# Optimization experiments

Measured on AMD Instinct MI355X. Metric: run time of the kernel, lower is better.

## Reference

```python
import jax, jax.numpy as jnp
import numpy as np

N = 30000   # nodes per graph batch
E = 480000  # edges per graph batch
G = 64      # number of graphs
IN = 20
D = 512
H = 4
C = D // H  # 128 per-head channels
HID = 128
EPS = 1e-5


def setup_inputs() -> dict:
    key = jax.random.key(0)
    ks = jax.random.split(key, 40)
    rn = lambda k, s, sc=0.05: jax.random.normal(k, s, jnp.float32) * sc
    inp = {}
    inp["wl_x"] = jax.random.normal(ks[0], (N, IN), jnp.float32)
    inp["mt_x"] = jax.random.normal(ks[1], (N, IN), jnp.float32)
    inp["wl_edge_index"] = jax.random.randint(ks[2], (2, E), 0, N)
    inp["mt_edge_index"] = jax.random.randint(ks[3], (2, E), 0, N)
    inp["wl_batch"] = jnp.sort(jax.random.randint(ks[4], (N,), 0, G))
    inp["mt_batch"] = jnp.sort(jax.random.randint(ks[5], (N,), 0, G))
    # GIN1 MLP: 20 -> 512 -> 512
    inp["gin1_W1"] = rn(ks[6], (IN, D)); inp["gin1_b1"] = jnp.zeros((D,), jnp.float32)
    inp["gin1_W2"] = rn(ks[7], (D, D)); inp["gin1_b2"] = jnp.zeros((D,), jnp.float32)
    inp["bn1_g"] = jnp.ones((D,), jnp.float32); inp["bn1_b"] = jnp.zeros((D,), jnp.float32)
    # GIN2 MLP: 512 -> 512 -> 512
    inp["gin2_W1"] = rn(ks[8], (D, D)); inp["gin2_b1"] = jnp.zeros((D,), jnp.float32)
    inp["gin2_W2"] = rn(ks[9], (D, D)); inp["gin2_b2"] = jnp.zeros((D,), jnp.float32)
    inp["bn2_g"] = jnp.ones((D,), jnp.float32); inp["bn2_b"] = jnp.zeros((D,), jnp.float32)
    # GAT: 512 -> 4 heads x 128, concat -> 512
    inp["gat_W"] = rn(ks[10], (D, H * C))
    inp["gat_as"] = rn(ks[11], (H, C))
    inp["gat_ad"] = rn(ks[12], (H, C))
    inp["gat_bias"] = jnp.zeros((H * C,), jnp.float32)
    # fc_wl: 512 -> 512 -> BN -> ReLU -> 128
    inp["fc_W1"] = rn(ks[13], (D, D)); inp["fc_b1"] = jnp.zeros((D,), jnp.float32)
    inp["fc_bn_g"] = jnp.ones((D,), jnp.float32); inp["fc_bn_b"] = jnp.zeros((D,), jnp.float32)
    inp["fc_W2"] = rn(ks[14], (D, HID)); inp["fc_b2"] = jnp.zeros((HID,), jnp.float32)
    inp["reg_W1"] = rn(ks[15], (2 * HID, HID)); inp["reg_b1"] = jnp.zeros((HID,), jnp.float32)
    inp["reg_W2"] = rn(ks[16], (HID, 1)); inp["reg_b2"] = jnp.zeros((1,), jnp.float32)
    return inp


def _bn(h, g, b):
    m = h.mean(0)
    v = h.var(0)
    return (h - m) * jax.lax.rsqrt(v + EPS) * g + b


def reference(wl_x, mt_x, wl_edge_index, mt_edge_index, wl_batch, mt_batch,
              gin1_W1, gin1_b1, gin1_W2, gin1_b2, bn1_g, bn1_b,
              gin2_W1, gin2_b1, gin2_W2, gin2_b2, bn2_g, bn2_b,
              gat_W, gat_as, gat_ad, gat_bias,
              fc_W1, fc_b1, fc_bn_g, fc_bn_b, fc_W2, fc_b2,
              reg_W1, reg_b1, reg_W2, reg_b2):
    def branch(x, ei, batch):
        n = x.shape[0]
        src, dst = ei[0], ei[1]
        # GIN1: nn((1+eps)*x + sum_{j->i} x_j), eps=0
        agg = jax.ops.segment_sum(x[src], dst, num_segments=n)
        h = x + agg
        h = jax.nn.relu(h @ gin1_W1 + gin1_b1) @ gin1_W2 + gin1_b2
        h = jax.nn.relu(_bn(h, bn1_g, bn1_b))
        # GIN2
        agg = jax.ops.segment_sum(h[src], dst, num_segments=n)
        h2 = h + agg
        h2 = jax.nn.relu(h2 @ gin2_W1 + gin2_b1) @ gin2_W2 + gin2_b2
        h2 = jax.nn.relu(_bn(h2, bn2_g, bn2_b))
        # GAT (adds self-loops, LeakyReLU(0.2), softmax over incoming edges)
        loop = jnp.arange(n)
        s2 = jnp.concatenate([src, loop])
        d2 = jnp.concatenate([dst, loop])
        hh = (h2 @ gat_W).reshape(n, H, C)           # [n,H,C]
        a_s = (hh * gat_as).sum(-1)                  # [n,H]
        a_d = (hh * gat_ad).sum(-1)                  # [n,H]
        e = jax.nn.leaky_relu(a_s[s2] + a_d[d2], 0.2)  # [E+n,H]
        mx = jax.ops.segment_max(e, d2, num_segments=n)
        ex = jnp.exp(e - mx[d2])
        den = jax.ops.segment_sum(ex, d2, num_segments=n)
        alpha = ex / den[d2]                          # [E+n,H]
        out = jax.ops.segment_sum(hh[s2] * alpha[:, :, None], d2,
                                  num_segments=n).reshape(n, H * C) + gat_bias
        # global add pool over graphs
        g = jax.ops.segment_sum(out, batch, num_segments=G)  # [G,512]
        # shared fc head
        g = jax.nn.relu(_bn(g @ fc_W1 + fc_b1, fc_bn_g, fc_bn_b)) @ fc_W2 + fc_b2
        return g                                       # [G,128]

    xw = branch(wl_x, wl_edge_index, wl_batch)
    xm = branch(mt_x, mt_edge_index, mt_batch)
    x = jnp.concatenate([xw, xm], axis=1)             # [G,256]
    ddg = (jax.nn.relu(x @ reg_W1 + reg_b1) @ reg_W2 + reg_b2)[:, 0]
    return ddg                                         # [G]
```

## Files before the change

kernel.cpp:

```cpp
#include <hip/hip_runtime.h>
#include <hip/hip_bf16.h>
#include <math.h>

#define N1     30000
#define NT     60000
#define E1     480000
#define NG     64
#define NGT    128
#define DIN    20
#define DD     512
#define NH     4
#define CH     128
#define NHID   128
#define PSPLIT 8
#define BN_EPS 1e-5f

typedef __attribute__((ext_vector_type(8))) short bf16x8;
typedef __attribute__((ext_vector_type(4))) float f32x4;
typedef __attribute__((address_space(1))) const void cg_void;
typedef __attribute__((address_space(3))) void lds_void;

__device__ inline unsigned short f2b(float f) {
    __hip_bfloat16 h = __float2bfloat16(f);
    return *(unsigned short*)&h;
}
__device__ inline float b2f(unsigned short u) {
    return __uint_as_float(((unsigned)u) << 16);
}

__global__ __launch_bounds__(256) void k_xmerge(const float* __restrict__ a,
                                                const float* __restrict__ b,
                                                float* __restrict__ xm) {
    int i = blockIdx.x * 256 + threadIdx.x;
    int tot = NT * DIN;
    if (i < tot) xm[i] = (i < N1 * DIN) ? a[i] : b[i - N1 * DIN];
}

__global__ __launch_bounds__(256) void k_bmerge(const int* __restrict__ a,
                                                const int* __restrict__ b,
                                                int* __restrict__ bm) {
    int i = blockIdx.x * 256 + threadIdx.x;
    if (i < NT) bm[i] = (i < N1) ? a[i] : b[i - N1] + NG;
}

__global__ __launch_bounds__(256) void k_hist2(const int* __restrict__ dwl,
                                               const int* __restrict__ dmt,
                                               int* __restrict__ cnt) {
    for (int e = blockIdx.x * blockDim.x + threadIdx.x; e < E1;
         e += gridDim.x * blockDim.x) {
        atomicAdd(&cnt[dwl[e]], 1);
        atomicAdd(&cnt[dmt[e] + N1], 1);
    }
}

__global__ __launch_bounds__(512) void k_scan2(const int* __restrict__ cnt,
                                               int* __restrict__ rowptr,
                                               int* __restrict__ cursor, int n) {
    __shared__ int sd[512];
    int t = threadIdx.x;
    int per = (n + 511) / 512;
    int lo = t * per, hi = lo + per;
    if (hi > n) hi = n;
    int s = 0;
    for (int i = lo; i < hi; ++i) s += cnt[i];
    sd[t] = s;
    __syncthreads();
    for (int off = 1; off < 512; off <<= 1) {
        int v = (t >= off) ? sd[t - off] : 0;
        __syncthreads();
        sd[t] += v;
        __syncthreads();
    }
    int run = sd[t] - s;
    for (int i = lo; i < hi; ++i) {
        rowptr[i] = run;
        cursor[i] = run;
        run += cnt[i];
    }
    if (t == 511) rowptr[n] = sd[511];
}

__global__ __launch_bounds__(256) void k_scatter2(const int* __restrict__ swl,
                                                  const int* __restrict__ dwl,
                                                  const int* __restrict__ smt,
                                                  const int* __restrict__ dmt,
                                                  int* __restrict__ cursor,
                                                  int* __restrict__ col) {
    for (int e = blockIdx.x * blockDim.x + threadIdx.x; e < E1;
         e += gridDim.x * blockDim.x) {
        int d0 = dwl[e];
        col[atomicAdd(&cursor[d0], 1)] = swl[e];
        int d1 = dmt[e] + N1;
        col[atomicAdd(&cursor[d1], 1)] = smt[e] + N1;
    }
}

__global__ __launch_bounds__(256) void k_wconv(const float* __restrict__ W,
                                               unsigned short* __restrict__ Wt) {
    int n = blockIdx.x;
    for (int k = threadIdx.x; k < DD; k += 256)
        Wt[n * DD + k] = f2b(W[k * DD + n]);
}

__global__ __launch_bounds__(256) void k_gin1_agg(const float* __restrict__ x,
                                                  const int* __restrict__ rowptr,
                                                  const int* __restrict__ col,
                                                  float* __restrict__ out) {
    int node = blockIdx.x * 4 + (threadIdx.x >> 6);
    int lane = threadIdx.x & 63;
    if (node >= NT) return;
    int p0 = rowptr[node], p1 = rowptr[node + 1];
    float acc = 0.f;
    if (lane < DIN) acc = x[(size_t)node * DIN + lane];
    for (int j = p0; j < p1; ++j) {
        int s = col[j];
        if (lane < DIN) acc += x[(size_t)s * DIN + lane];
    }
    if (lane < DIN) out[(size_t)node * DIN + lane] = acc;
}

__global__ __launch_bounds__(256) void k_gemm20(const float* __restrict__ A,
                                                const float* __restrict__ W,
                                                const float* __restrict__ bias,
                                                unsigned short* __restrict__ C) {
    __shared__ float Ws[DIN][128];
    __shared__ float As[64][DIN + 1];
    int t = threadIdx.x;
    int row0 = blockIdx.x * 64;
    int col0 = blockIdx.y * 128;
    for (int i = t; i < DIN * 128; i += 256) {
        int k = i >> 7, c = i & 127;
        Ws[k][c] = W[k * DD + col0 + c];
    }
    for (int i = t; i < 64 * DIN; i += 256) {
        int r = i / DIN, k = i % DIN;
        int rr = row0 + r;
        if (rr >= NT) rr = NT - 1;
        As[r][k] = A[(size_t)rr * DIN + k];
    }
    __syncthreads();
    int c4 = (t & 31) * 4;
    int r0 = (t >> 5) * 8;
    float acc[8][4];
#pragma unroll
    for (int i = 0; i < 8; i++)
#pragma unroll
        for (int j = 0; j < 4; j++) acc[i][j] = 0.f;
    for (int k = 0; k < DIN; k++) {
        float4 b = *(const float4*)&Ws[k][c4];
#pragma unroll
        for (int i = 0; i < 8; i++) {
            float a = As[r0 + i][k];
            acc[i][0] += a * b.x; acc[i][1] += a * b.y;
            acc[i][2] += a * b.z; acc[i][3] += a * b.w;
        }
    }
    float4 bb = *(const float4*)&bias[col0 + c4];
#pragma unroll
    for (int i = 0; i < 8; i++) {
        int r = row0 + r0 + i;
        if (r < NT) {
            short4 o;
            o.x = (short)f2b(fmaxf(acc[i][0] + bb.x, 0.f));
            o.y = (short)f2b(fmaxf(acc[i][1] + bb.y, 0.f));
            o.z = (short)f2b(fmaxf(acc[i][2] + bb.z, 0.f));
            o.w = (short)f2b(fmaxf(acc[i][3] + bb.w, 0.f));
            *(short4*)&C[(size_t)r * DD + col0 + c4] = o;
        }
    }
}

template <int MODE>
__global__ __launch_bounds__(256) void k_gemm_mfma(
    const unsigned short* __restrict__ A, const unsigned short* __restrict__ Wt,
    const float* __restrict__ bias, unsigned short* __restrict__ Cb,
    const float* __restrict__ att_s, const float* __restrict__ att_d,
    float* __restrict__ as_o, float* __restrict__ ad_o, int M) {
    __shared__ unsigned short lds[2 * 128 * 64];
    __shared__ float s_att[2 * 128];
    unsigned short* AsU = lds;
    unsigned short* BsU = lds + 128 * 64;

    int t = threadIdx.x;
    int lane = t & 63;
    int w = t >> 6;
    int wr = w >> 1, wc = w & 1;
    int bid = blockIdx.x;
    int row0 = (bid >> 2) * 128;
    int ct = bid & 3;
    int col0 = ct * 128;

    int l8 = lane >> 3;
    int swz = (lane & 7) ^ l8;

    f32x4 acc[4][4];
#pragma unroll
    for (int i = 0; i < 4; i++)
#pragma unroll
        for (int j = 0; j < 4; j++) acc[i][j] = (f32x4){0.f, 0.f, 0.f, 0.f};

    int fr = lane & 15, fq = lane >> 4, f7 = lane & 7;

    for (int s = 0; s < 8; ++s) {
        int k0 = s * 64;
        __syncthreads();
#pragma unroll
        for (int q = 0; q < 4; q++) {
            int rl = w * 32 + q * 8 + l8;
            int gr = row0 + rl;
            if (gr >= M) gr = M - 1;
            const unsigned short* srcA = A + (size_t)gr * DD + k0 + swz * 8;
            unsigned short* dstA = AsU + (w * 32 + q * 8) * 64;
            __builtin_amdgcn_global_load_lds((cg_void*)srcA, (lds_void*)dstA,
                                             16, 0, 0);
            int cl = w * 32 + q * 8 + l8;
            const unsigned short* srcB = Wt + (size_t)(col0 + cl) * DD + k0 +
                                         swz * 8;
            unsigned short* dstB = BsU + (w * 32 + q * 8) * 64;
            __builtin_amdgcn_global_load_lds((cg_void*)srcB, (lds_void*)dstB,
                                             16, 0, 0);
        }
        __syncthreads();
#pragma unroll
        for (int kk = 0; kk < 2; kk++) {
            bf16x8 am[4], bn[4];
#pragma unroll
            for (int i = 0; i < 4; i++) {
                int row = wr * 64 + i * 16 + fr;
                int ks = (kk * 4 + fq) ^ f7;
                am[i] = *(const bf16x8*)&AsU[row * 64 + ks * 8];
            }
#pragma unroll
            for (int j = 0; j < 4; j++) {
                int row = wc * 64 + j * 16 + fr;
                int ks = (kk * 4 + fq) ^ f7;
                bn[j] = *(const bf16x8*)&BsU[row * 64 + ks * 8];
            }
#pragma unroll
            for (int i = 0; i < 4; i++)
#pragma unroll
                for (int j = 0; j < 4; j++)
                    acc[i][j] = __builtin_amdgcn_mfma_f32_16x16x32_bf16(
                        am[i], bn[j], acc[i][j], 0, 0, 0);
        }
    }

    __syncthreads();
    unsigned short* st = lds;
    if (MODE == 2) {
        if (t < 128) { s_att[t] = 0.f; s_att[128 + t] = 0.f; }
    }
    __syncthreads();

    float bv[4], fa[4], fd[4];
#pragma unroll
    for (int j = 0; j < 4; j++) {
        int c = wc * 64 + j * 16 + fr;
        if (MODE == 2) {
            fa[j] = att_s[ct * CH + c];
            fd[j] = att_d[ct * CH + c];
        } else {
            bv[j] = bias[col0 + c];
        }
    }
#pragma unroll
    for (int i = 0; i < 4; i++) {
#pragma unroll
        for (int r = 0; r < 4; r++) {
            int lrow = wr * 64 + i * 16 + fq * 4 + r;
            float ss = 0.f, sd = 0.f;
#pragma unroll
            for (int j = 0; j < 4; j++) {
                float v = acc[i][j][r];
                if (MODE != 2) {
                    v += bv[j];
                    if (MODE == 1) v = fmaxf(v, 0.f);
                } else {
                    ss += v * fa[j];
                    sd += v * fd[j];
                }
                st[lrow * 128 + wc * 64 + j * 16 + fr] = f2b(v);
            }
            if (MODE == 2) {
                atomicAdd(&s_att[lrow], ss);
                atomicAdd(&s_att[128 + lrow], sd);
            }
        }
    }
    __syncthreads();
#pragma unroll
    for (int i = 0; i < 8; i++) {
        int idx = i * 256 + t;
        int row = idx >> 4, seg = idx & 15;
        int grow = row0 + row;
        if (grow < M) {
            int4 v = *(const int4*)&st[row * 128 + seg * 8];
            *(int4*)&Cb[(size_t)grow * DD + col0 + seg * 8] = v;
        }
    }
    if (MODE == 2 && t < 128) {
        int grow = row0 + t;
        if (grow < M) {
            as_o[grow * NH + ct] = s_att[t];
            ad_o[grow * NH + ct] = s_att[128 + t];
        }
    }
}

__global__ __launch_bounds__(256) void k_bn_stats2b(const unsigned short* __restrict__ h,
                                                    float* __restrict__ sums) {
    int t = threadIdx.x;
    float sa[2] = {0.f, 0.f}, qa[2] = {0.f, 0.f};
    float sb[2] = {0.f, 0.f}, qb[2] = {0.f, 0.f};
    for (int r = blockIdx.x; r < NT; r += gridDim.x) {
        unsigned u = ((const unsigned*)(h + (size_t)r * DD))[t];
        float va = b2f((unsigned short)(u & 0xffff));
        float vb = b2f((unsigned short)(u >> 16));
        int seg = (r >= N1);
        sa[seg] += va; qa[seg] += va * va;
        sb[seg] += vb; qb[seg] += vb * vb;
    }
    int c = 2 * t;
#pragma unroll
    for (int seg = 0; seg < 2; ++seg) {
        atomicAdd(&sums[seg * DD + c], sa[seg]);
        atomicAdd(&sums[seg * DD + c + 1], sb[seg]);
        atomicAdd(&sums[2 * DD + seg * DD + c], qa[seg]);
        atomicAdd(&sums[2 * DD + seg * DD + c + 1], qb[seg]);
    }
}

__global__ __launch_bounds__(512) void k_bn_fin2(const float* __restrict__ sums,
                                                 const float* __restrict__ g,
                                                 const float* __restrict__ b,
                                                 float* __restrict__ sc) {
    int c = threadIdx.x;
#pragma unroll
    for (int seg = 0; seg < 2; ++seg) {
        float mean = sums[seg * DD + c] / (float)N1;
        float var = sums[2 * DD + seg * DD + c] / (float)N1 - mean * mean;
        float rs = rsqrtf(var + BN_EPS);
        float s = g[c] * rs;
        sc[seg * DD + c] = s;
        sc[2 * DD + seg * DD + c] = b[c] - mean * s;
    }
}

__global__ __launch_bounds__(256) void k_bn_apply_ip(unsigned short* __restrict__ h,
                                                     const float* __restrict__ sc) {
    int total = NT * (DD / 8);
    for (int i = blockIdx.x * blockDim.x + threadIdx.x; i < total;
         i += gridDim.x * blockDim.x) {
        int4 v = ((int4*)h)[i];
        unsigned short* u = (unsigned short*)&v;
        int row = i >> 6;
        int seg = (row >= N1);
        int c = (i & 63) * 8;
        const float* scale = sc + seg * DD;
        const float* shift = sc + 2 * DD + seg * DD;
#pragma unroll
        for (int k = 0; k < 8; k++) {
            float f = b2f(u[k]) * scale[c + k] + shift[c + k];
            u[k] = f2b(fmaxf(f, 0.f));
        }
        ((int4*)h)[i] = v;
    }
}

__global__ __launch_bounds__(256) void k_agg512b(const unsigned short* __restrict__ h,
                                                 const int* __restrict__ rowptr,
                                                 const int* __restrict__ col,
                                                 unsigned short* __restrict__ out) {
    int node = blockIdx.x * 4 + (threadIdx.x >> 6);
    int lane = threadIdx.x & 63;
    if (node >= NT) return;
    size_t base = (size_t)node * DD + lane * 8;
    float acc[8];
    {
        int4 v = *(const int4*)&h[base];
        const unsigned short* u = (const unsigned short*)&v;
#pragma unroll
        for (int i = 0; i < 8; i++) acc[i] = b2f(u[i]);
    }
    int p0 = rowptr[node], p1 = rowptr[node + 1];
    int j = p0;
    for (; j + 1 < p1; j += 2) {
        int s0 = col[j], s1 = col[j + 1];
        int4 v0 = *(const int4*)&h[(size_t)s0 * DD + lane * 8];
        int4 v1 = *(const int4*)&h[(size_t)s1 * DD + lane * 8];
        const unsigned short* u0 = (const unsigned short*)&v0;
        const unsigned short* u1 = (const unsigned short*)&v1;
#pragma unroll
        for (int i = 0; i < 8; i++) acc[i] += b2f(u0[i]) + b2f(u1[i]);
    }
    if (j < p1) {
        int4 v0 = *(const int4*)&h[(size_t)col[j] * DD + lane * 8];
        const unsigned short* u0 = (const unsigned short*)&v0;
#pragma unroll
        for (int i = 0; i < 8; i++) acc[i] += b2f(u0[i]);
    }
    int4 o;
    unsigned short* uo = (unsigned short*)&o;
#pragma unroll
    for (int i = 0; i < 8; i++) uo[i] = f2b(acc[i]);
    *(int4*)&out[base] = o;
}

__global__ __launch_bounds__(256) void k_gat_gather(
    const unsigned short* __restrict__ hh, const float* __restrict__ a_s,
    const float* __restrict__ a_d, const int* __restrict__ rowptr,
    const int* __restrict__ col, unsigned short* __restrict__ outB) {
    int node = blockIdx.x * 4 + (threadIdx.x >> 6);
    int lane = threadIdx.x & 63;
    if (node >= NT) return;
    int h = lane >> 4;
    int idx4 = node * NH + h;
    float adi = a_d[idx4];
    float e = a_s[idx4] + adi;
    e = (e > 0.f) ? e : 0.2f * e;
    float ws = __expf(e);
    float den = ws;
    float acc[8];
    {
        int4 v = *(const int4*)&hh[(size_t)node * DD + lane * 8];
        const unsigned short* u = (const unsigned short*)&v;
#pragma unroll
        for (int i = 0; i < 8; i++) acc[i] = ws * b2f(u[i]);
    }
    int p0 = rowptr[node], p1 = rowptr[node + 1];
    int j = p0;
    for (; j + 1 < p1; j += 2) {
        int s0 = col[j], s1 = col[j + 1];
        float e0 = a_s[s0 * NH + h] + adi;
        float e1 = a_s[s1 * NH + h] + adi;
        e0 = (e0 > 0.f) ? e0 : 0.2f * e0;
        e1 = (e1 > 0.f) ? e1 : 0.2f * e1;
        float w0 = __expf(e0), w1 = __expf(e1);
        int4 v0 = *(const int4*)&hh[(size_t)s0 * DD + lane * 8];
        int4 v1 = *(const int4*)&hh[(size_t)s1 * DD + lane * 8];
        const unsigned short* u0 = (const unsigned short*)&v0;
        const unsigned short* u1 = (const unsigned short*)&v1;
#pragma unroll
        for (int i = 0; i < 8; i++) acc[i] += w0 * b2f(u0[i]) + w1 * b2f(u1[i]);
        den += w0 + w1;
    }
    if (j < p1) {
        int s0 = col[j];
        float e0 = a_s[s0 * NH + h] + adi;
        e0 = (e0 > 0.f) ? e0 : 0.2f * e0;
        float w0 = __expf(e0);
        int4 v0 = *(const int4*)&hh[(size_t)s0 * DD + lane * 8];
        const unsigned short* u0 = (const unsigned short*)&v0;
#pragma unroll
        for (int i = 0; i < 8; i++) acc[i] += w0 * b2f(u0[i]);
        den += w0;
    }
    float inv = 1.f / den;
    int4 o;
    unsigned short* uo = (unsigned short*)&o;
#pragma unroll
    for (int i = 0; i < 8; i++) uo[i] = f2b(acc[i] * inv);
    *(int4*)&outB[(size_t)node * DD + lane * 8] = o;
}

__device__ inline void graph_range(const int* __restrict__ bm, int g,
                                   int& start, int& end) {
    int lo = 0, hi = NT;
    while (lo < hi) { int m = (lo + hi) >> 1; if (bm[m] < g) lo = m + 1; else hi = m; }
    start = lo;
    hi = NT;
    while (lo < hi) { int m = (lo + hi) >> 1; if (bm[m] < g + 1) lo = m + 1; else hi = m; }
    end = lo;
}

__global__ __launch_bounds__(256) void k_pool1(const unsigned short* __restrict__ gatout,
                                               const int* __restrict__ bm,
                                               float* __restrict__ partial) {
    int g = blockIdx.x;
    int s = blockIdx.y;
    int t = threadIdx.x;
    int start, end;
    graph_range(bm, g, start, end);
    float a0 = 0.f, a1 = 0.f;
    for (int n = start + s; n < end; n += PSPLIT) {
        unsigned u = ((const unsigned*)(gatout + (size_t)n * DD))[t];
        a0 += b2f((unsigned short)(u & 0xffff));
        a1 += b2f((unsigned short)(u >> 16));
    }
    float* p = partial + ((size_t)g * PSPLIT + s) * DD;
    p[2 * t] = a0;
    p[2 * t + 1] = a1;
}

__global__ __launch_bounds__(512) void k_pool2(const float* __restrict__ partial,
                                               const int* __restrict__ bm,
                                               const float* __restrict__ bias,
                                               float* __restrict__ pool) {
    int g = blockIdx.x;
    int c = threadIdx.x;
    int start, end;
    graph_range(bm, g, start, end);
    float acc = 0.f;
#pragma unroll
    for (int s = 0; s < PSPLIT; ++s)
        acc += partial[((size_t)g * PSPLIT + s) * DD + c];
    pool[g * DD + c] = acc + (float)(end - start) * bias[c];
}

__global__ __launch_bounds__(256) void k_fc1(const float* __restrict__ gin,
                                             const float* __restrict__ W,
                                             const float* __restrict__ bias,
                                             float* __restrict__ out) {
    __shared__ float row[DD];
    int g = blockIdx.x;
    int t = threadIdx.x;
    row[t] = gin[g * DD + t];
    row[t + 256] = gin[g * DD + t + 256];
    __syncthreads();
    for (int cc = 0; cc < 2; ++cc) {
        int c = t + cc * 256;
        float acc = 0.f;
        for (int k = 0; k < DD; k++) acc += row[k] * W[k * DD + c];
        out[g * DD + c] = acc + bias[c];
    }
}

__global__ __launch_bounds__(512) void k_bn64_2(float* __restrict__ h,
                                                const float* __restrict__ g_,
                                                const float* __restrict__ b_) {
    int c = threadIdx.x;
#pragma unroll
    for (int seg = 0; seg < 2; ++seg) {
        float s = 0.f, q = 0.f;
        for (int r = 0; r < NG; r++) {
            float v = h[(seg * NG + r) * DD + c];
            s += v; q += v * v;
        }
        float mean = s / (float)NG;
        float var = q / (float)NG - mean * mean;
        float rs = rsqrtf(var + BN_EPS);
        float sc = g_[c] * rs, sh = b_[c] - mean * sc;
        for (int r = 0; r < NG; r++) {
            float v = h[(seg * NG + r) * DD + c];
            h[(seg * NG + r) * DD + c] = fmaxf(v * sc + sh, 0.f);
        }
    }
}

__global__ __launch_bounds__(128) void k_fc2(const float* __restrict__ h,
                                             const float* __restrict__ W,
                                             const float* __restrict__ bias,
                                             float* __restrict__ out) {
    __shared__ float row[DD];
    int g = blockIdx.x;
    int t = threadIdx.x;
    for (int i = t; i < DD; i += 128) row[i] = h[g * DD + i];
    __syncthreads();
    float acc = 0.f;
    for (int k = 0; k < DD; k++) acc += row[k] * W[k * NHID + t];
    out[g * NHID + t] = acc + bias[t];
}

__global__ __launch_bounds__(128) void k_reg(const float* __restrict__ gout,
                                             const float* __restrict__ W1,
                                             const float* __restrict__ b1,
                                             const float* __restrict__ W2,
                                             const float* __restrict__ b2,
                                             float* __restrict__ out) {
    __shared__ float x[256];
    __shared__ float red[128];
    int g = blockIdx.x;
    int t = threadIdx.x;
    x[t] = gout[g * NHID + t];
    x[t + 128] = gout[(NG + g) * NHID + t];
    __syncthreads();
    float acc = b1[t];
    for (int k = 0; k < 256; k++) acc += x[k] * W1[k * NHID + t];
    acc = fmaxf(acc, 0.f);
    red[t] = acc * W2[t];
    __syncthreads();
    for (int off = 64; off; off >>= 1) {
        if (t < off) red[t] += red[t + off];
        __syncthreads();
    }
    if (t == 0) out[g] = red[0] + b2[0];
}

extern "C" void kernel_launch(void* const* d_in, const int* in_sizes, int n_in,
                              void* d_out, int out_size, void* d_ws, size_t ws_size,
                              hipStream_t stream) {
    const float* wl_x = (const float*)d_in[0];
    const float* mt_x = (const float*)d_in[1];
    const int* wl_ei = (const int*)d_in[2];
    const int* mt_ei = (const int*)d_in[3];
    const int* wl_batch = (const int*)d_in[4];
    const int* mt_batch = (const int*)d_in[5];
    const float* gin1_W1 = (const float*)d_in[6];
    const float* gin1_b1 = (const float*)d_in[7];
    const float* gin1_W2 = (const float*)d_in[8];
    const float* gin1_b2 = (const float*)d_in[9];
    const float* bn1_g = (const float*)d_in[10];
    const float* bn1_b = (const float*)d_in[11];
    const float* gin2_W1 = (const float*)d_in[12];
    const float* gin2_b1 = (const float*)d_in[13];
    const float* gin2_W2 = (const float*)d_in[14];
    const float* gin2_b2 = (const float*)d_in[15];
    const float* bn2_g = (const float*)d_in[16];
    const float* bn2_b = (const float*)d_in[17];
    const float* gat_W = (const float*)d_in[18];
    const float* gat_as = (const float*)d_in[19];
    const float* gat_ad = (const float*)d_in[20];
    const float* gat_bias = (const float*)d_in[21];
    const float* fc_W1 = (const float*)d_in[22];
    const float* fc_b1 = (const float*)d_in[23];
    const float* fc_bn_g = (const float*)d_in[24];
    const float* fc_bn_b = (const float*)d_in[25];
    const float* fc_W2 = (const float*)d_in[26];
    const float* fc_b2 = (const float*)d_in[27];
    const float* reg_W1 = (const float*)d_in[28];
    const float* reg_b1 = (const float*)d_in[29];
    const float* reg_W2 = (const float*)d_in[30];
    const float* reg_b2 = (const float*)d_in[31];
    float* out = (float*)d_out;

    char* ws = (char*)d_ws;
    size_t o = 0;
    auto alloc = [&](size_t bytes) {
        size_t r = o;
        o = (o + bytes + 255) & ~(size_t)255;
        return r;
    };
    unsigned short* hbA = (unsigned short*)(ws + alloc((size_t)NT * DD * 2));
    unsigned short* hbB = (unsigned short*)(ws + alloc((size_t)NT * DD * 2));
    float* xm = (float*)(ws + alloc((size_t)NT * DIN * 4));
    float* bufA = (float*)(ws + alloc((size_t)NT * DIN * 4));
    int* bm = (int*)(ws + alloc((size_t)NT * 4));
    int* cnt = (int*)(ws + alloc((size_t)NT * 4));
    int* rowptr = (int*)(ws + alloc((size_t)(NT + 1) * 4));
    int* cursor = (int*)(ws + alloc((size_t)NT * 4));
    int* colidx = (int*)(ws + alloc((size_t)2 * E1 * 4));
    float* a_s = (float*)(ws + alloc((size_t)NT * NH * 4));
    float* a_d = (float*)(ws + alloc((size_t)NT * NH * 4));
    float* bnsums = (float*)(ws + alloc(4 * DD * 4));
    float* bnsc = (float*)(ws + alloc(4 * DD * 4));
    float* partial = (float*)(ws + alloc((size_t)NGT * PSPLIT * DD * 4));
    float* pool = (float*)(ws + alloc((size_t)NGT * DD * 4));
    float* fch = (float*)(ws + alloc((size_t)NGT * DD * 4));
    float* gout = (float*)(ws + alloc((size_t)NGT * NHID * 4));
    unsigned short* Wt1 = (unsigned short*)(ws + alloc((size_t)DD * DD * 2));
    unsigned short* Wt2 = (unsigned short*)(ws + alloc((size_t)DD * DD * 2));
    unsigned short* Wt3 = (unsigned short*)(ws + alloc((size_t)DD * DD * 2));
    unsigned short* Wt4 = (unsigned short*)(ws + alloc((size_t)DD * DD * 2));
    (void)ws_size; (void)in_sizes; (void)n_in; (void)out_size;

    k_wconv<<<DD, 256, 0, stream>>>(gin1_W2, Wt1);
    k_wconv<<<DD, 256, 0, stream>>>(gin2_W1, Wt2);
    k_wconv<<<DD, 256, 0, stream>>>(gin2_W2, Wt3);
    k_wconv<<<DD, 256, 0, stream>>>(gat_W, Wt4);
    k_xmerge<<<(NT * DIN + 255) / 256, 256, 0, stream>>>(wl_x, mt_x, xm);
    k_bmerge<<<(NT + 255) / 256, 256, 0, stream>>>(wl_batch, mt_batch, bm);

    hipMemsetAsync(cnt, 0, (size_t)NT * 4, stream);
    k_hist2<<<512, 256, 0, stream>>>(wl_ei + E1, mt_ei + E1, cnt);
    k_scan2<<<1, 512, 0, stream>>>(cnt, rowptr, cursor, NT);
    k_scatter2<<<512, 256, 0, stream>>>(wl_ei, wl_ei + E1, mt_ei, mt_ei + E1,
                                        cursor, colidx);

    int gmm = ((NT + 127) / 128) * 4;
    dim3 g20((NT + 63) / 64, 4);

    auto bnpass = [&](unsigned short* buf, const float* g, const float* b) {
        hipMemsetAsync(bnsums, 0, 4 * DD * 4, stream);
        k_bn_stats2b<<<256, 256, 0, stream>>>(buf, bnsums);
        k_bn_fin2<<<1, 512, 0, stream>>>(bnsums, g, b, bnsc);
        k_bn_apply_ip<<<2048, 256, 0, stream>>>(buf, bnsc);
    };

    k_gin1_agg<<<(NT + 3) / 4, 256, 0, stream>>>(xm, rowptr, colidx, bufA);
    k_gemm20<<<g20, 256, 0, stream>>>(bufA, gin1_W1, gin1_b1, hbA);
    k_gemm_mfma<0><<<gmm, 256, 0, stream>>>(hbA, Wt1, gin1_b2, hbB, nullptr,
                                            nullptr, nullptr, nullptr, NT);
    bnpass(hbB, bn1_g, bn1_b);

    k_agg512b<<<(NT + 3) / 4, 256, 0, stream>>>(hbB, rowptr, colidx, hbA);
    k_gemm_mfma<1><<<gmm, 256, 0, stream>>>(hbA, Wt2, gin2_b1, hbB, nullptr,
                                            nullptr, nullptr, nullptr, NT);
    k_gemm_mfma<0><<<gmm, 256, 0, stream>>>(hbB, Wt3, gin2_b2, hbA, nullptr,
                                            nullptr, nullptr, nullptr, NT);
    bnpass(hbA, bn2_g, bn2_b);

    k_gemm_mfma<2><<<gmm, 256, 0, stream>>>(hbA, Wt4, nullptr, hbB, gat_as,
                                            gat_ad, a_s, a_d, NT);
    k_gat_gather<<<(NT + 3) / 4, 256, 0, stream>>>(hbB, a_s, a_d, rowptr, colidx,
                                                   hbA);
    k_pool1<<<dim3(NGT, PSPLIT), 256, 0, stream>>>(hbA, bm, partial);
    k_pool2<<<NGT, 512, 0, stream>>>(partial, bm, gat_bias, pool);

    k_fc1<<<NGT, 256, 0, stream>>>(pool, fc_W1, fc_b1, fch);
    k_bn64_2<<<1, 512, 0, stream>>>(fch, fc_bn_g, fc_bn_b);
    k_fc2<<<NGT, 128, 0, stream>>>(fch, fc_W2, fc_b2, gout);

    k_reg<<<NG, 128, 0, stream>>>(gout, reg_W1, reg_b1, reg_W2, reg_b2, out);
}
```

Baseline: 1.417 ms.

## Fuse BN1 apply into GIN2 aggregation and widen MFMA GEMM tile to 256 rows

The first BatchNorm apply pass is dropped. The scale/shift plus ReLU is now applied on the fly inside the 512-wide neighbor aggregation, which saves one full read-modify-write of the 60000x512 activation buffer. The MFMA GEMM now computes a 256x128 tile per block, with each wave owning 64 rows across all 128 columns. This halves the number of times each weight column tile is loaded and gives more MFMAs per LDS read, at the cost of twice the accumulator registers and larger LDS. Per-edge aggregation now re-applies BN on every gathered neighbor, which adds ALU work to a memory-bound kernel.

New measurement: 1.470 ms. 1.04x slower.

```diff
diff --git a/kernel.cpp b/kernel.cpp
--- a/kernel.cpp
+++ b/kernel.cpp
@@ -176,28 +176,26 @@
     const float* __restrict__ bias, unsigned short* __restrict__ Cb,
     const float* __restrict__ att_s, const float* __restrict__ att_d,
     float* __restrict__ as_o, float* __restrict__ ad_o, int M) {
-    __shared__ unsigned short lds[2 * 128 * 64];
-    __shared__ float s_att[2 * 128];
-    unsigned short* AsU = lds;
-    unsigned short* BsU = lds + 128 * 64;
+    __shared__ unsigned short AsU[256 * 64];
+    __shared__ unsigned short BsU[128 * 64];
+    __shared__ float s_att[2 * 256];
 
     int t = threadIdx.x;
     int lane = t & 63;
     int w = t >> 6;
-    int wr = w >> 1, wc = w & 1;
     int bid = blockIdx.x;
-    int row0 = (bid >> 2) * 128;
+    int row0 = (bid >> 2) * 256;
     int ct = bid & 3;
     int col0 = ct * 128;
 
     int l8 = lane >> 3;
     int swz = (lane & 7) ^ l8;
 
-    f32x4 acc[4][4];
+    f32x4 acc[4][8];
 #pragma unroll
     for (int i = 0; i < 4; i++)
 #pragma unroll
-        for (int j = 0; j < 4; j++) acc[i][j] = (f32x4){0.f, 0.f, 0.f, 0.f};
+        for (int j = 0; j < 8; j++) acc[i][j] = (f32x4){0.f, 0.f, 0.f, 0.f};
 
     int fr = lane & 15, fq = lane >> 4, f7 = lane & 7;
 
@@ -205,57 +203,55 @@
         int k0 = s * 64;
         __syncthreads();
 #pragma unroll
-        for (int q = 0; q < 4; q++) {
-            int rl = w * 32 + q * 8 + l8;
-            int gr = row0 + rl;
+        for (int q = 0; q < 8; q++) {
+            int rowbase = w * 64 + q * 8;
+            int gr = row0 + rowbase + l8;
             if (gr >= M) gr = M - 1;
             const unsigned short* srcA = A + (size_t)gr * DD + k0 + swz * 8;
-            unsigned short* dstA = AsU + (w * 32 + q * 8) * 64;
-            __builtin_amdgcn_global_load_lds((cg_void*)srcA, (lds_void*)dstA,
+            __builtin_amdgcn_global_load_lds((cg_void*)srcA,
+                                             (lds_void*)(AsU + rowbase * 64),
                                              16, 0, 0);
-            int cl = w * 32 + q * 8 + l8;
-            const unsigned short* srcB = Wt + (size_t)(col0 + cl) * DD + k0 +
-                                         swz * 8;
-            unsigned short* dstB = BsU + (w * 32 + q * 8) * 64;
-            __builtin_amdgcn_global_load_lds((cg_void*)srcB, (lds_void*)dstB,
+        }
+#pragma unroll
+        for (int q = 0; q < 4; q++) {
+            int rowbase = w * 32 + q * 8;
+            const unsigned short* srcB = Wt +
+                (size_t)(col0 + rowbase + l8) * DD + k0 + swz * 8;
+            __builtin_amdgcn_global_load_lds((cg_void*)srcB,
+                                             (lds_void*)(BsU + rowbase * 64),
                                              16, 0, 0);
         }
         __syncthreads();
 #pragma unroll
         for (int kk = 0; kk < 2; kk++) {
-            bf16x8 am[4], bn[4];
+            bf16x8 am[4], bn[8];
 #pragma unroll
             for (int i = 0; i < 4; i++) {
-                int row = wr * 64 + i * 16 + fr;
+                int row = w * 64 + i * 16 + fr;
                 int ks = (kk * 4 + fq) ^ f7;
                 am[i] = *(const bf16x8*)&AsU[row * 64 + ks * 8];
             }
 #pragma unroll
-            for (int j = 0; j < 4; j++) {
-                int row = wc * 64 + j * 16 + fr;
+            for (int j = 0; j < 8; j++) {
+                int row = j * 16 + fr;
                 int ks = (kk * 4 + fq) ^ f7;
                 bn[j] = *(const bf16x8*)&BsU[row * 64 + ks * 8];
             }
 #pragma unroll
             for (int i = 0; i < 4; i++)
 #pragma unroll
-                for (int j = 0; j < 4; j++)
+                for (int j = 0; j < 8; j++)
                     acc[i][j] = __builtin_amdgcn_mfma_f32_16x16x32_bf16(
                         am[i], bn[j], acc[i][j], 0, 0, 0);
         }
     }
 
     __syncthreads();
-    unsigned short* st = lds;
-    if (MODE == 2) {
-        if (t < 128) { s_att[t] = 0.f; s_att[128 + t] = 0.f; }
-    }
-    __syncthreads();
-
-    float bv[4], fa[4], fd[4];
-#pragma unroll
-    for (int j = 0; j < 4; j++) {
-        int c = wc * 64 + j * 16 + fr;
+    unsigned short* st = AsU;
+    float bv[8], fa[8], fd[8];
+#pragma unroll
+    for (int j = 0; j < 8; j++) {
+        int c = j * 16 + fr;
         if (MODE == 2) {
             fa[j] = att_s[ct * CH + c];
             fd[j] = att_d[ct * CH + c];
@@ -263,46 +259,64 @@
             bv[j] = bias[col0 + c];
         }
     }
-#pragma unroll
-    for (int i = 0; i < 4; i++) {
-#pragma unroll
-        for (int r = 0; r < 4; r++) {
-            int lrow = wr * 64 + i * 16 + fq * 4 + r;
-            float ss = 0.f, sd = 0.f;
-#pragma unroll
-            for (int j = 0; j < 4; j++) {
-                float v = acc[i][j][r];
-                if (MODE != 2) {
-                    v += bv[j];
-                    if (MODE == 1) v = fmaxf(v, 0.f);
-                } else {
-                    ss += v * fa[j];
-                    sd += v * fd[j];
+    if (MODE == 2) { s_att[t] = 0.f; s_att[256 + t] = 0.f; }
+    __syncthreads();
+    if (MODE == 2) {
+#pragma unroll
+        for (int i = 0; i < 4; i++) {
+#pragma unroll
+            for (int r = 0; r < 4; r++) {
+                int lrow = w * 64 + i * 16 + fq * 4 + r;
+                float ss = 0.f, sd = 0.f;
+#pragma unroll
+                for (int j = 0; j < 8; j++) {
+                    ss += acc[i][j][r] * fa[j];
+                    sd += acc[i][j][r] * fd[j];
                 }
-                st[lrow * 128 + wc * 64 + j * 16 + fr] = f2b(v);
+                atomicAdd(&s_att[lrow], ss);
+                atomicAdd(&s_att[256 + lrow], sd);
             }
-            if (MODE == 2) {
-                atomicAdd(&s_att[lrow], ss);
-                atomicAdd(&s_att[128 + lrow], sd);
+        }
+    }
+#pragma unroll
+    for (int h = 0; h < 2; h++) {
+        if ((w >> 1) == h) {
+            int lr0 = (w & 1) * 64;
+#pragma unroll
+            for (int i = 0; i < 4; i++) {
+#pragma unroll
+                for (int r = 0; r < 4; r++) {
+                    int lrow = lr0 + i * 16 + fq * 4 + r;
+#pragma unroll
+                    for (int j = 0; j < 8; j++) {
+                        float v = acc[i][j][r];
+                        if (MODE != 2) {
+                            v += bv[j];
+                            if (MODE == 1) v = fmaxf(v, 0.f);
+                        }
+                        st[lrow * 128 + j * 16 + fr] = f2b(v);
+                    }
+                }
             }
         }
-    }
-    __syncthreads();
-#pragma unroll
-    for (int i = 0; i < 8; i++) {
-        int idx = i * 256 + t;
-        int row = idx >> 4, seg = idx & 15;
-        int grow = row0 + row;
-        if (grow < M) {
-            int4 v = *(const int4*)&st[row * 128 + seg * 8];
-            *(int4*)&Cb[(size_t)grow * DD + col0 + seg * 8] = v;
-        }
-    }
-    if (MODE == 2 && t < 128) {
+        __syncthreads();
+#pragma unroll
+        for (int i = 0; i < 8; i++) {
+            int idx = i * 256 + t;
+            int row = idx >> 4, seg = idx & 15;
+            int grow = row0 + h * 128 + row;
+            if (grow < M) {
+                int4 v = *(const int4*)&st[row * 128 + seg * 8];
+                *(int4*)&Cb[(size_t)grow * DD + col0 + seg * 8] = v;
+            }
+        }
+        __syncthreads();
+    }
+    if (MODE == 2) {
         int grow = row0 + t;
         if (grow < M) {
             as_o[grow * NH + ct] = s_att[t];
-            ad_o[grow * NH + ct] = s_att[128 + t];
+            ad_o[grow * NH + ct] = s_att[256 + t];
         }
     }
 }
@@ -367,37 +381,50 @@
     }
 }
 
-__global__ __launch_bounds__(256) void k_agg512b(const unsigned short* __restrict__ h,
+__global__ __launch_bounds__(256) void k_agg512f(const unsigned short* __restrict__ h,
                                                  const int* __restrict__ rowptr,
                                                  const int* __restrict__ col,
+                                                 const float* __restrict__ sc,
                                                  unsigned short* __restrict__ out) {
     int node = blockIdx.x * 4 + (threadIdx.x >> 6);
     int lane = threadIdx.x & 63;
     if (node >= NT) return;
-    size_t base = (size_t)node * DD + lane * 8;
+    int seg = (node >= N1);
+    int cb = lane * 8;
+    float scl[8], shf[8];
+    *(float4*)&scl[0] = *(const float4*)&sc[seg * DD + cb];
+    *(float4*)&scl[4] = *(const float4*)&sc[seg * DD + cb + 4];
+    *(float4*)&shf[0] = *(const float4*)&sc[2 * DD + seg * DD + cb];
+    *(float4*)&shf[4] = *(const float4*)&sc[2 * DD + seg * DD + cb + 4];
+
+    size_t base = (size_t)node * DD + cb;
     float acc[8];
     {
         int4 v = *(const int4*)&h[base];
         const unsigned short* u = (const unsigned short*)&v;
 #pragma unroll
-        for (int i = 0; i < 8; i++) acc[i] = b2f(u[i]);
+        for (int i = 0; i < 8; i++)
+            acc[i] = fmaxf(b2f(u[i]) * scl[i] + shf[i], 0.f);
     }
     int p0 = rowptr[node], p1 = rowptr[node + 1];
     int j = p0;
     for (; j + 1 < p1; j += 2) {
         int s0 = col[j], s1 = col[j + 1];
-        int4 v0 = *(const int4*)&h[(size_t)s0 * DD + lane * 8];
-        int4 v1 = *(const int4*)&h[(size_t)s1 * DD + lane * 8];
+        int4 v0 = *(const int4*)&h[(size_t)s0 * DD + cb];
+        int4 v1 = *(const int4*)&h[(size_t)s1 * DD + cb];
         const unsigned short* u0 = (const unsigned short*)&v0;
         const unsigned short* u1 = (const unsigned short*)&v1;
 #pragma unroll
-        for (int i = 0; i < 8; i++) acc[i] += b2f(u0[i]) + b2f(u1[i]);
+        for (int i = 0; i < 8; i++)
+            acc[i] += fmaxf(b2f(u0[i]) * scl[i] + shf[i], 0.f) +
+                      fmaxf(b2f(u1[i]) * scl[i] + shf[i], 0.f);
     }
     if (j < p1) {
-        int4 v0 = *(const int4*)&h[(size_t)col[j] * DD + lane * 8];
+        int4 v0 = *(const int4*)&h[(size_t)col[j] * DD + cb];
         const unsigned short* u0 = (const unsigned short*)&v0;
 #pragma unroll
-        for (int i = 0; i < 8; i++) acc[i] += b2f(u0[i]);
+        for (int i = 0; i < 8; i++)
+            acc[i] += fmaxf(b2f(u0[i]) * scl[i] + shf[i], 0.f);
     }
     int4 o;
     unsigned short* uo = (unsigned short*)&o;
@@ -666,28 +693,26 @@
     k_scatter2<<<512, 256, 0, stream>>>(wl_ei, wl_ei + E1, mt_ei, mt_ei + E1,
                                         cursor, colidx);
 
-    int gmm = ((NT + 127) / 128) * 4;
+    int gmm = ((NT + 255) / 256) * 4;
     dim3 g20((NT + 63) / 64, 4);
-
-    auto bnpass = [&](unsigned short* buf, const float* g, const float* b) {
-        hipMemsetAsync(bnsums, 0, 4 * DD * 4, stream);
-        k_bn_stats2b<<<256, 256, 0, stream>>>(buf, bnsums);
-        k_bn_fin2<<<1, 512, 0, stream>>>(bnsums, g, b, bnsc);
-        k_bn_apply_ip<<<2048, 256, 0, stream>>>(buf, bnsc);
-    };
 
     k_gin1_agg<<<(NT + 3) / 4, 256, 0, stream>>>(xm, rowptr, colidx, bufA);
     k_gemm20<<<g20, 256, 0, stream>>>(bufA, gin1_W1, gin1_b1, hbA);
     k_gemm_mfma<0><<<gmm, 256, 0, stream>>>(hbA, Wt1, gin1_b2, hbB, nullptr,
                                             nullptr, nullptr, nullptr, NT);
-    bnpass(hbB, bn1_g, bn1_b);
-
-    k_agg512b<<<(NT + 3) / 4, 256, 0, stream>>>(hbB, rowptr, colidx, hbA);
+    hipMemsetAsync(bnsums, 0, 4 * DD * 4, stream);
+    k_bn_stats2b<<<256, 256, 0, stream>>>(hbB, bnsums);
+    k_bn_fin2<<<1, 512, 0, stream>>>(bnsums, bn1_g, bn1_b, bnsc);
+
+    k_agg512f<<<(NT + 3) / 4, 256, 0, stream>>>(hbB, rowptr, colidx, bnsc, hbA);
     k_gemm_mfma<1><<<gmm, 256, 0, stream>>>(hbA, Wt2, gin2_b1, hbB, nullptr,
                                             nullptr, nullptr, nullptr, NT);
     k_gemm_mfma<0><<<gmm, 256, 0, stream>>>(hbB, Wt3, gin2_b2, hbA, nullptr,
                                             nullptr, nullptr, nullptr, NT);
-    bnpass(hbA, bn2_g, bn2_b);
+    hipMemsetAsync(bnsums, 0, 4 * DD * 4, stream);
+    k_bn_stats2b<<<256, 256, 0, stream>>>(hbA, bnsums);
+    k_bn_fin2<<<1, 512, 0, stream>>>(bnsums, bn2_g, bn2_b, bnsc);
+    k_bn_apply_ip<<<2048, 256, 0, stream>>>(hbA, bnsc);
 
     k_gemm_mfma<2><<<gmm, 256, 0, stream>>>(hbA, Wt4, nullptr, hbB, gat_as,
                                             gat_ad, a_s, a_d, NT);
```
